# Optimization experiments

Measured on AMD Instinct MI355X. Metric: run time of the kernel, lower is better.

The kernel has to match this reference:

```python
import jax, jax.numpy as jnp
import numpy as np

B, T, C, H = 2, 2048, 1024, 16
D = C // H  # head dim = 64


def setup_inputs() -> dict:
    key = jax.random.key(0)
    k1, k2, k3 = jax.random.split(key, 3)
    x = jax.random.normal(k1, (B, T, C), dtype=jnp.float32)
    w_attn = jax.random.normal(k2, (C, 3 * C), dtype=jnp.float32) * (1.0 / np.sqrt(C))
    b_attn = jnp.zeros((3 * C,), dtype=jnp.float32)
    w_proj = jax.random.normal(k3, (C, C), dtype=jnp.float32) * (1.0 / np.sqrt(C))
    b_proj = jnp.zeros((C,), dtype=jnp.float32)
    return {"x": x, "w_attn": w_attn, "b_attn": b_attn, "w_proj": w_proj, "b_proj": b_proj}


def reference(x, w_attn, b_attn, w_proj, b_proj):
    Bx, Tx, Cx = x.shape
    qkv = x @ w_attn + b_attn  # [B, T, 3C]
    q, k, v = jnp.split(qkv, 3, axis=-1)
    # [B, H, T, D]
    q = q.reshape(Bx, Tx, H, D).swapaxes(1, 2)
    k = k.reshape(Bx, Tx, H, D).swapaxes(1, 2)
    v = v.reshape(Bx, Tx, H, D).swapaxes(1, 2)
    scale = 1.0 / jnp.sqrt(jnp.float32(D))
    att = jnp.einsum('bhqd,bhkd->bhqk', q, k) * scale  # [B, H, T, T]
    causal = jnp.tril(jnp.ones((Tx, Tx), dtype=bool))
    att = jnp.where(causal[None, None], att, -jnp.inf)
    att = jax.nn.softmax(att, axis=-1)
    y = jnp.einsum('bhqk,bhkd->bhqd', att, v)  # [B, H, T, D]
    y = y.swapaxes(1, 2).reshape(Bx, Tx, Cx)
    return y @ w_proj + b_proj
```

## Files before the change

kernel.cpp:

```cpp
#include <hip/hip_runtime.h>
#include <hip/hip_bf16.h>


typedef __attribute__((ext_vector_type(8))) short short8x;
typedef __attribute__((ext_vector_type(4))) float float4x;
typedef __attribute__((ext_vector_type(4))) unsigned short ushort4x;
typedef __attribute__((ext_vector_type(2))) unsigned int uint2x;

#define MFMA_BF16 __builtin_amdgcn_mfma_f32_16x16x32_bf16

typedef const __attribute__((address_space(1))) void gvoid_t;
typedef __attribute__((address_space(3))) void lvoid_t;
#define GLOAD_LDS16(g, l) __builtin_amdgcn_global_load_lds((gvoid_t*)(g), (lvoid_t*)(l), 16, 0, 0)

__device__ __forceinline__ unsigned short f2b(float f) {
    unsigned int u = __float_as_uint(f);
    u = (u + 0x7FFFu + ((u >> 16) & 1u)) >> 16;
    return (unsigned short)u;
}
__device__ __forceinline__ unsigned int pk2(float a, float b) {
    return __builtin_amdgcn_perm(__float_as_uint(b) + 0x8000u,
                                 __float_as_uint(a) + 0x8000u, 0x07060302u);
}

__device__ __forceinline__ void stage32(const unsigned short* g, size_t rs,
                                        short* ldst, int w0, int lane) {
    const int r8 = lane >> 3;
    const int sc = ((lane & 7) ^ r8) * 8;
#pragma unroll
    for (int q = 0; q < 4; q++) {
        GLOAD_LDS16(g + (size_t)(w0 + q * 8 + r8) * rs + sc,
                    ldst + (w0 + q * 8) * 64);
    }
}

__global__ __launch_bounds__(256) void prep(const float* __restrict__ x,
                                            unsigned short* __restrict__ xb,
                                            const float* __restrict__ wa,
                                            unsigned short* __restrict__ waT,
                                            const float* __restrict__ wp,
                                            unsigned short* __restrict__ wpT) {
    __shared__ float tile[32][33];
    const int bid = blockIdx.x;
    const int tid = threadIdx.x;
    if (bid < 4096) {
        int i = bid * 256 + tid;
        float4 v = ((const float4*)x)[i];
        ushort4x o = { f2b(v.x), f2b(v.y), f2b(v.z), f2b(v.w) };
        ((ushort4x*)xb)[i] = o;
        return;
    }
    int b2 = bid - 4096;
    const float* in;
    unsigned short* outp;
    int cols, bx, by;
    if (b2 < 3072) { in = wa; outp = waT; cols = 3072; bx = b2 % 96; by = b2 / 96; }
    else { b2 -= 3072; in = wp; outp = wpT; cols = 1024; bx = b2 & 31; by = b2 >> 5; }
    const int tx = tid & 31, ty = tid >> 5;
    const int cbase = bx * 32, rbase = by * 32;
    const int c = cbase + tx;
    for (int j = 0; j < 32; j += 8)
        tile[ty + j][tx] = in[(size_t)(rbase + ty + j) * cols + c];
    __syncthreads();
    const int rr = rbase + tx;
    for (int j = 0; j < 32; j += 8) {
        int cc = cbase + ty + j;
        outp[(size_t)cc * 1024 + rr] = f2b(tile[tx][ty + j]);
    }
}

__global__ __launch_bounds__(256) void gemm_qkv(const unsigned short* __restrict__ A,
                                                const unsigned short* __restrict__ BT,
                                                const float* __restrict__ bias,
                                                unsigned short* __restrict__ QK,
                                                unsigned short* __restrict__ VTg) {
    __shared__ union {
        struct { short A[128 * 64]; short B[128 * 64]; } s;
        short vt[4][64 * 80];
    } lds;

    const int K = 1024;
    const int lane = threadIdx.x & 63;
    const int wave = threadIdx.x >> 6;
    const int quad = lane >> 4;
    const int l16  = lane & 15;
    const int sw   = l16 & 7;

    const int rblk = blockIdx.y * 128;
    const int cblk = blockIdx.x * 128;
    const int wr = wave >> 1, wc = wave & 1;

    float4x acc[4][4] = {};

    const unsigned short* Ag = A  + (size_t)rblk * K;
    const unsigned short* Bg = BT + (size_t)cblk * K;

    for (int kk = 0; kk < K; kk += 64) {
        stage32(Ag + kk, K, lds.s.A, wave * 32, lane);
        stage32(Bg + kk, K, lds.s.B, wave * 32, lane);
        __syncthreads();

#pragma unroll
        for (int kk2 = 0; kk2 < 2; kk2++) {
            short8x a[4], b[4];
#pragma unroll
            for (int i = 0; i < 4; i++)
                a[i] = *(const short8x*)&lds.s.A[(wr * 64 + i * 16 + l16) * 64 +
                                                 ((kk2 * 4 + quad) ^ sw) * 8];
#pragma unroll
            for (int j = 0; j < 4; j++)
                b[j] = *(const short8x*)&lds.s.B[(wc * 64 + j * 16 + l16) * 64 +
                                                 ((kk2 * 4 + quad) ^ sw) * 8];
#pragma unroll
            for (int i = 0; i < 4; i++)
#pragma unroll
                for (int j = 0; j < 4; j++)
                    acc[i][j] = MFMA_BF16(a[i], b[j], acc[i][j], 0, 0, 0);
        }
        __syncthreads();
    }

    const int rbase = rblk + wr * 64;
    const int cbase = cblk + wc * 64;

    if (cbase < 2048) {
        const float QS = 0.18033688f;
#pragma unroll
        for (int i = 0; i < 4; i++) {
#pragma unroll
            for (int j = 0; j < 4; j++) {
                int c = cbase + j * 16 + l16;
                float bv = bias[c];
                float sc = (c < 1024) ? QS : 1.0f;
#pragma unroll
                for (int reg = 0; reg < 4; reg++) {
                    int r = rbase + i * 16 + quad * 4 + reg;
                    QK[(size_t)r * 2048 + c] = f2b((acc[i][j][reg] + bv) * sc);
                }
            }
        }
    } else {
#pragma unroll
        for (int i = 0; i < 4; i++) {
#pragma unroll
            for (int j = 0; j < 4; j++) {
                int c = cbase + j * 16 + l16;
                float bv = bias[c];
                uint2x p = { pk2(acc[i][j][0] + bv, acc[i][j][1] + bv),
                             pk2(acc[i][j][2] + bv, acc[i][j][3] + bv) };
                *(uint2x*)&lds.vt[wave][(j * 16 + l16) * 80 + i * 16 + quad * 4] = p;
            }
        }
        const int h   = (cbase - 2048) >> 6;
        const int hb  = (rbase >> 11) * 16 + h;
        const int tb0 = rbase & 2047;
#pragma unroll
        for (int p = 0; p < 8; p++) {
            int dd   = p * 8 + (lane >> 3);
            int toff = (lane & 7) * 8;
            short8x vv = *(const short8x*)&lds.vt[wave][dd * 80 + toff];
            *(short8x*)&VTg[((size_t)(hb * 64 + dd)) * 2048 + tb0 + toff] = vv;
        }
    }
}

__global__ __launch_bounds__(256) void gemm_proj(const unsigned short* __restrict__ A,
                                                 const unsigned short* __restrict__ BT,
                                                 const float* __restrict__ bias,
                                                 float* __restrict__ out) {
    __shared__ struct { short A[64 * 64]; short B[64 * 64]; } lds;

    const int K = 1024, N = 1024;
    const int lane = threadIdx.x & 63;
    const int wave = threadIdx.x >> 6;
    const int quad = lane >> 4;
    const int l16  = lane & 15;
    const int sw   = l16 & 7;

    const int rblk = blockIdx.y * 64;
    const int cblk = blockIdx.x * 64;

    float4x acc[4] = {};

    const unsigned short* Ag = A  + (size_t)rblk * K;
    const unsigned short* Bg = BT + (size_t)cblk * K;

    for (int kk = 0; kk < K; kk += 64) {
        if (wave < 2) stage32(Ag + kk, K, lds.A, wave * 32, lane);
        else          stage32(Bg + kk, K, lds.B, (wave - 2) * 32, lane);
        __syncthreads();

#pragma unroll
        for (int kk2 = 0; kk2 < 2; kk2++) {
            short8x bfr = *(const short8x*)&lds.B[(wave * 16 + l16) * 64 +
                                                  ((kk2 * 4 + quad) ^ sw) * 8];
#pragma unroll
            for (int i = 0; i < 4; i++) {
                short8x a = *(const short8x*)&lds.A[(i * 16 + l16) * 64 +
                                                    ((kk2 * 4 + quad) ^ sw) * 8];
                acc[i] = MFMA_BF16(a, bfr, acc[i], 0, 0, 0);
            }
        }
        __syncthreads();
    }

    const int c = cblk + wave * 16 + l16;
    const float bv = bias[c];
#pragma unroll
    for (int i = 0; i < 4; i++) {
#pragma unroll
        for (int reg = 0; reg < 4; reg++) {
            int r = rblk + i * 16 + quad * 4 + reg;
            out[(size_t)r * N + c] = acc[i][reg] + bv;
        }
    }
}

__global__ __launch_bounds__(256, 8) void attn_kernel(const unsigned short* __restrict__ QK,
                                                      const unsigned short* __restrict__ VT,
                                                      unsigned short* __restrict__ Y) {
    __shared__ __attribute__((aligned(16))) short Kl[2][32 * 64];
    __shared__ __attribute__((aligned(16))) short Vl[2][64 * 32];
    __shared__ __attribute__((aligned(16))) short Pl[4][16 * 32];

    const int tid  = threadIdx.x;
    const int lane = tid & 63;
    const int wave = tid >> 6;
    const int quad = lane >> 4;
    const int l16  = lane & 15;
    const int sw3  = l16 & 3;
    const int sw7  = l16 & 7;

    const int level = blockIdx.x >> 5;
    const int bh    = blockIdx.x & 31;
    const int pair  = level >> 1;
    const int qb    = (level & 1) ? pair : (31 - pair);
    const int b = bh >> 4, h = bh & 15;

    const unsigned short* Qp = QK + ((size_t)b * 2048) * 2048 + h * 64;
    const unsigned short* Kp = Qp + 1024;
    const unsigned short* Vp = VT + (size_t)bh * 64 * 2048;

    const int qbase = qb * 64 + wave * 16;
    const int kend  = qbase + 16;
    const int ntb   = 2 * qb + 2;

    short8x aq[2];
#pragma unroll
    for (int kk = 0; kk < 2; kk++)
        aq[kk] = *(const short8x*)(Qp + (size_t)(qbase + l16) * 2048 + kk * 32 + quad * 8);

    short8x ones;
#pragma unroll
    for (int e = 0; e < 8; e++) ones[e] = (short)0x3F80;

    const int krow = wave * 8 + (lane >> 3);
    const unsigned short* Kg = Kp + (size_t)krow * 2048 + ((lane & 7) ^ (lane >> 3)) * 8;
    const int vrow = wave * 16 + (lane >> 2);
    const unsigned short* Vg = Vp + (size_t)vrow * 2048 + (((lane & 3) ^ ((lane >> 2) & 3)) * 8);

    GLOAD_LDS16(Kg, &Kl[0][wave * 8 * 64]);
    GLOAD_LDS16(Vg, &Vl[0][wave * 16 * 32]);
    __syncthreads();

    float4x O[4] = {};
    float4x lacc = {};

    for (int it = 0; it < ntb; it++) {
        const int kb = it * 32;
        const short* Kc = Kl[it & 1];
        const short* Vc = Vl[it & 1];

        if (it + 1 < ntb) {
            GLOAD_LDS16(Kg + (size_t)(kb + 32) * 2048, &Kl[(it + 1) & 1][wave * 8 * 64]);
            GLOAD_LDS16(Vg + (kb + 32), &Vl[(it + 1) & 1][wave * 16 * 32]);
        }

        if (kb < kend) {
            float4x S[2];
#pragma unroll
            for (int t = 0; t < 2; t++) {
                short8x kf0 = *(const short8x*)&Kc[(t * 16 + l16) * 64 + ((quad) ^ sw7) * 8];
                short8x kf1 = *(const short8x*)&Kc[(t * 16 + l16) * 64 + ((4 + quad) ^ sw7) * 8];
                S[t] = (float4x){0.f, 0.f, 0.f, 0.f};
                S[t] = MFMA_BF16(kf0, aq[0], S[t], 0, 0, 0);
                S[t] = MFMA_BF16(kf1, aq[1], S[t], 0, 0, 0);
            }

            if (kb + 32 > qbase) {
                int q = qbase + l16;
#pragma unroll
                for (int t = 0; t < 2; t++)
#pragma unroll
                    for (int reg = 0; reg < 4; reg++)
                        if (kb + t * 16 + quad * 4 + reg > q) S[t][reg] = -1e38f;
            }

#pragma unroll
            for (int t = 0; t < 2; t++) {
                float e0 = __builtin_amdgcn_exp2f(S[t][0]);
                float e1 = __builtin_amdgcn_exp2f(S[t][1]);
                float e2 = __builtin_amdgcn_exp2f(S[t][2]);
                float e3 = __builtin_amdgcn_exp2f(S[t][3]);
                uint2x p = { pk2(e0, e1), pk2(e2, e3) };
                *(uint2x*)&Pl[wave][l16 * 32 + ((t * 2 + (quad >> 1)) ^ sw3) * 8 + (quad & 1) * 4] = p;
            }

            short8x bp = *(const short8x*)&Pl[wave][l16 * 32 + (quad ^ sw3) * 8];
            lacc = MFMA_BF16(ones, bp, lacc, 0, 0, 0);
#pragma unroll
            for (int dt = 0; dt < 4; dt++) {
                short8x vf = *(const short8x*)&Vc[(dt * 16 + l16) * 32 + (quad ^ sw3) * 8];
                O[dt] = MFMA_BF16(vf, bp, O[dt], 0, 0, 0);
            }
        }
        __syncthreads();
    }

    float rl = 1.0f / lacc[0];
    short* scr = &Kl[0][0] + wave * 1024;
#pragma unroll
    for (int dt = 0; dt < 4; dt++) {
        uint2x o = { pk2(O[dt][0] * rl, O[dt][1] * rl),
                     pk2(O[dt][2] * rl, O[dt][3] * rl) };
        *(uint2x*)&scr[l16 * 64 + ((2 * dt + (quad >> 1)) ^ sw7) * 8 + (quad & 1) * 4] = o;
    }
    const int t = qbase + l16;
#pragma unroll
    for (int cc = 0; cc < 2; cc++) {
        short8x row = *(const short8x*)&scr[l16 * 64 + ((2 * quad + cc) ^ sw7) * 8];
        *(short8x*)&Y[((size_t)(b * 2048 + t)) * 1024 + h * 64 + (2 * quad + cc) * 8] = row;
    }
}

extern "C" void kernel_launch(void* const* d_in, const int* in_sizes, int n_in,
                              void* d_out, int out_size, void* d_ws, size_t ws_size,
                              hipStream_t stream) {
    const float* x      = (const float*)d_in[0];
    const float* w_attn = (const float*)d_in[1];
    const float* b_attn = (const float*)d_in[2];
    const float* w_proj = (const float*)d_in[3];
    const float* b_proj = (const float*)d_in[4];
    float* out = (float*)d_out;

    char* ws = (char*)d_ws;
    unsigned short* xb  = (unsigned short*)(ws + (size_t)0);
    unsigned short* waT = (unsigned short*)(ws + (size_t)(8  << 20));
    unsigned short* wpT = (unsigned short*)(ws + (size_t)(14 << 20));
    unsigned short* QKb = (unsigned short*)(ws + (size_t)(16 << 20));
    unsigned short* VTb = (unsigned short*)(ws + (size_t)(32 << 20));
    unsigned short* yb  = (unsigned short*)(ws + (size_t)(40 << 20));

    prep<<<8192, 256, 0, stream>>>(x, xb, w_attn, waT, w_proj, wpT);

    gemm_qkv<<<dim3(24, 32), 256, 0, stream>>>(xb, waT, b_attn, QKb, VTb);

    attn_kernel<<<1024, 256, 0, stream>>>(QKb, VTb, yb);

    gemm_proj<<<dim3(16, 64), 256, 0, stream>>>(yb, wpT, b_proj, out);
}
```

Baseline: 200.1 us.

## Load V in 64-key tiles and replace ones-MFMA row-sum with shuffles

V^T tiles are now fetched 64 keys wide (128-byte rows, two loads per thread) every other iteration, double-buffered separately from K, with an XOR swizzle matching the K layout. This is meant to give wider, more coalesced global-to-LDS transfers and fewer load issues. The row-sum MFMA against a ones vector is replaced by scalar accumulation of the exponentials plus two cross-lane shuffles at the end, and the launch-bounds occupancy hint of 8 is dropped. In exchange, V shared memory grows from 8 KB to 16 KB, which may lower occupancy. The scalar sum also uses the fp32 exponentials rather than their bf16-rounded values.

Result: faster. 191.2 us (-4.4%).

```diff
diff --git a/kernel.cpp b/kernel.cpp
--- a/kernel.cpp
+++ b/kernel.cpp
@@ -216,11 +216,11 @@
     }
 }
 
-__global__ __launch_bounds__(256, 8) void attn_kernel(const unsigned short* __restrict__ QK,
-                                                      const unsigned short* __restrict__ VT,
-                                                      unsigned short* __restrict__ Y) {
+__global__ __launch_bounds__(256) void attn_kernel(const unsigned short* __restrict__ QK,
+                                                   const unsigned short* __restrict__ VT,
+                                                   unsigned short* __restrict__ Y) {
     __shared__ __attribute__((aligned(16))) short Kl[2][32 * 64];
-    __shared__ __attribute__((aligned(16))) short Vl[2][64 * 32];
+    __shared__ __attribute__((aligned(16))) short Vl[2][64 * 64];
     __shared__ __attribute__((aligned(16))) short Pl[4][16 * 32];
 
     const int tid  = threadIdx.x;
@@ -244,36 +244,40 @@
     const int qbase = qb * 64 + wave * 16;
     const int kend  = qbase + 16;
     const int ntb   = 2 * qb + 2;
+    const int nvw   = qb + 1;
 
     short8x aq[2];
 #pragma unroll
     for (int kk = 0; kk < 2; kk++)
         aq[kk] = *(const short8x*)(Qp + (size_t)(qbase + l16) * 2048 + kk * 32 + quad * 8);
 
-    short8x ones;
-#pragma unroll
-    for (int e = 0; e < 8; e++) ones[e] = (short)0x3F80;
-
-    const int krow = wave * 8 + (lane >> 3);
-    const unsigned short* Kg = Kp + (size_t)krow * 2048 + ((lane & 7) ^ (lane >> 3)) * 8;
-    const int vrow = wave * 16 + (lane >> 2);
-    const unsigned short* Vg = Vp + (size_t)vrow * 2048 + (((lane & 3) ^ ((lane >> 2) & 3)) * 8);
-
-    GLOAD_LDS16(Kg, &Kl[0][wave * 8 * 64]);
-    GLOAD_LDS16(Vg, &Vl[0][wave * 16 * 32]);
+    const int kRow = tid >> 3;
+    const int kOff = ((tid & 7) ^ (kRow & 7)) * 8;
+    const unsigned short* Ksrc = Kp + (size_t)kRow * 2048 + kOff;
+    const unsigned short* Vsrc0 = Vp + (size_t)kRow * 2048 + kOff;
+    const unsigned short* Vsrc1 = Vp + (size_t)(kRow + 32) * 2048 + kOff;
+
+    GLOAD_LDS16(Ksrc, &Kl[0][wave * 512]);
+    GLOAD_LDS16(Vsrc0, &Vl[0][wave * 512]);
+    GLOAD_LDS16(Vsrc1, &Vl[0][2048 + wave * 512]);
     __syncthreads();
 
+    float l = 0.f;
     float4x O[4] = {};
-    float4x lacc = {};
 
     for (int it = 0; it < ntb; it++) {
         const int kb = it * 32;
         const short* Kc = Kl[it & 1];
-        const short* Vc = Vl[it & 1];
-
-        if (it + 1 < ntb) {
-            GLOAD_LDS16(Kg + (size_t)(kb + 32) * 2048, &Kl[(it + 1) & 1][wave * 8 * 64]);
-            GLOAD_LDS16(Vg + (kb + 32), &Vl[(it + 1) & 1][wave * 16 * 32]);
+        const short* Vc = Vl[(it >> 1) & 1];
+        const int vh = (it & 1) * 4;
+
+        if (it + 1 < ntb)
+            GLOAD_LDS16(Ksrc + (size_t)(kb + 32) * 2048, &Kl[(it + 1) & 1][wave * 512]);
+        if (!(it & 1) && (it >> 1) + 1 < nvw) {
+            const int keyb = ((it >> 1) + 1) * 64;
+            short* vd = Vl[((it >> 1) + 1) & 1];
+            GLOAD_LDS16(Vsrc0 + keyb, &vd[wave * 512]);
+            GLOAD_LDS16(Vsrc1 + keyb, &vd[2048 + wave * 512]);
         }
 
         if (kb < kend) {
@@ -302,22 +306,25 @@
                 float e1 = __builtin_amdgcn_exp2f(S[t][1]);
                 float e2 = __builtin_amdgcn_exp2f(S[t][2]);
                 float e3 = __builtin_amdgcn_exp2f(S[t][3]);
+                l += (e0 + e1) + (e2 + e3);
                 uint2x p = { pk2(e0, e1), pk2(e2, e3) };
                 *(uint2x*)&Pl[wave][l16 * 32 + ((t * 2 + (quad >> 1)) ^ sw3) * 8 + (quad & 1) * 4] = p;
             }
 
             short8x bp = *(const short8x*)&Pl[wave][l16 * 32 + (quad ^ sw3) * 8];
-            lacc = MFMA_BF16(ones, bp, lacc, 0, 0, 0);
 #pragma unroll
             for (int dt = 0; dt < 4; dt++) {
-                short8x vf = *(const short8x*)&Vc[(dt * 16 + l16) * 32 + (quad ^ sw3) * 8];
+                short8x vf = *(const short8x*)&Vc[(dt * 16 + l16) * 64 + ((vh + quad) ^ sw7) * 8];
                 O[dt] = MFMA_BF16(vf, bp, O[dt], 0, 0, 0);
             }
         }
         __syncthreads();
     }
 
-    float rl = 1.0f / lacc[0];
+    float lv = l;
+    lv += __shfl_xor(lv, 16, 64);
+    lv += __shfl_xor(lv, 32, 64);
+    float rl = 1.0f / lv;
     short* scr = &Kl[0][0] + wave * 1024;
 #pragma unroll
     for (int dt = 0; dt < 4; dt++) {
```
